# Kernel tuning notes

Measured on AMD Instinct MI355X. Metric: run time of the kernel, lower is better.

## Reference

```python
import jax, jax.numpy as jnp
import numpy as np
import math

N, CIN, DM, H, W = 4, 64, 32, 64, 64
KH = KW = 3

def setup_inputs() -> dict:
    key = jax.random.key(0)
    ks = jax.random.split(key, 12)
    sc = 0.05
    return {
        "h": jax.random.normal(ks[0], (N, CIN, H, W), jnp.float32),
        "m": jax.random.normal(ks[1], (N, CIN, H, W), jnp.float32),
        "Wh": jax.random.normal(ks[2], (3 * DM, CIN), jnp.float32) * sc,
        "bh": jax.random.normal(ks[3], (3 * DM,), jnp.float32) * sc,
        "Wm": jax.random.normal(ks[4], (2 * DM, CIN), jnp.float32) * sc,
        "bm": jax.random.normal(ks[5], (2 * DM,), jnp.float32) * sc,
        "Wz": jax.random.normal(ks[6], (DM, 2 * DM), jnp.float32) * sc,
        "bz": jax.random.normal(ks[7], (DM,), jnp.float32) * sc,
        "Wo": jax.random.normal(ks[8], (3 * CIN, CIN + DM, KH, KW), jnp.float32) * sc,
        "bo": jax.random.normal(ks[9], (3 * CIN,), jnp.float32) * sc,
    }

def _conv1x1(x, Wt, b):
    # x: [N,Ci,H,W], Wt: [Co,Ci] -> [N,Co,H,W]
    return jnp.einsum('oi,nihw->nohw', Wt, x) + b[None, :, None, None]

def _attend(q, k, v):
    # q,k,v: [N,C,S]; out: [N,C,S]
    C = q.shape[1]
    scores = jnp.einsum('ncs,nct->nst', q, k) / math.sqrt(C)  # [N,S,S]
    attn = jax.nn.softmax(scores, axis=-1)
    return jnp.einsum('nst,nct->ncs', attn, v)

def reference(h, m, Wh, bh, Wm, bm, Wz, bz, Wo, bo):
    n, _, hh, ww = h.shape
    S = hh * ww
    hq, hk, hv = jnp.split(_conv1x1(h, Wh, bh), 3, axis=1)
    mk, mv = jnp.split(_conv1x1(m, Wm, bm), 2, axis=1)
    hq = hq.reshape(n, DM, S)
    hk = hk.reshape(n, DM, S)
    hv = hv.reshape(n, DM, S)
    mk = mk.reshape(n, DM, S)
    mv = mv.reshape(n, DM, S)
    Zh = _attend(hq, hk, hv).reshape(n, DM, hh, ww)
    Zm = _attend(hq, mk, mv).reshape(n, DM, hh, ww)
    Z = _conv1x1(jnp.concatenate([Zh, Zm], axis=1), Wz, bz)
    x = jnp.concatenate([Z, h], axis=1)  # [N, DM+CIN, H, W]
    out = jax.lax.conv_general_dilated(
        x, Wo, window_strides=(1, 1), padding='SAME',
        dimension_numbers=('NCHW', 'OIHW', 'NCHW')) + bo[None, :, None, None]
    i, g, o = jnp.split(out, 3, axis=1)
    i = jax.nn.sigmoid(i)
    g = jnp.tanh(g)
    m_next = i * g + (1.0 - i) * m
    h_next = jax.nn.sigmoid(o) * m_next
    return (h_next, m_next)
```

## Files before the change

kernel.cpp:

```cpp
#include <hip/hip_runtime.h>
#include <math.h>

#define NB 4
#define CIN 64
#define DM 32
#define S 4096
#define NW 4

#define OFF_Q  0
#define OFF_KH 262144
#define OFF_VH 524288
#define OFF_KM 786432
#define OFF_VM 1048576
#define OFF_ZH 1310720
#define OFF_ZM 1572864
#define OFF_WF 1835008

typedef __attribute__((ext_vector_type(8))) short bf16x8;
typedef __attribute__((ext_vector_type(4))) short s16x4;
typedef __attribute__((ext_vector_type(4))) float f32x4;
typedef __attribute__((ext_vector_type(2))) unsigned int u32x2;
typedef __attribute__((ext_vector_type(4))) unsigned int u32x4;

__device__ inline unsigned short f2b(float x) {
  union { float f; unsigned u; } v;
  v.f = x;
  unsigned r = (v.u + 0x7FFF + ((v.u >> 16) & 1)) >> 16;
  return (unsigned short)r;
}

__device__ inline float b2f(unsigned short u) {
  union { unsigned u; float f; } v;
  v.u = ((unsigned)u) << 16;
  return v.f;
}

__device__ inline unsigned fbits(float x) {
  union { float f; unsigned u; } v;
  v.f = x;
  return v.u;
}

__global__ __launch_bounds__(256) void prep_kernel(
    const float* __restrict__ h, const float* __restrict__ m,
    const float* __restrict__ Wh, const float* __restrict__ bh,
    const float* __restrict__ Wm, const float* __restrict__ bm,
    const float* __restrict__ Wo, float* __restrict__ ws) {
  __shared__ unsigned short sm[64][34];
  int bid = blockIdx.x;
  int tid = threadIdx.x;

  if (bid >= 512) {
    int idx = (bid - 512) * 256 + tid;
    int f = idx >> 8;
    int r = idx & 255;
    int lane = r >> 2;
    int jp = (r & 3) * 2;
    int ql = lane & 15, quad = lane >> 4;
    int co = (f / 27) * 16 + ql;
    int k = (f % 27) * 32 + quad * 8 + jp;
    int tap = k / 96;
    int ci = k - tap * 96;
    float a = Wo[((size_t)co * 96 + ci) * 9 + tap];
    float b = Wo[((size_t)co * 96 + ci + 1) * 9 + tap];
    unsigned val = (unsigned)f2b(a) | ((unsigned)f2b(b) << 16);
    ((unsigned*)(ws + OFF_WF))[idx] = val;
    return;
  }

  int mode = (bid >= 256) ? 1 : 0;
  const float* in = mode ? m : h;
  const float* W = mode ? Wm : Wh;
  const float* b = mode ? bm : bh;
  int lbid = bid & 255;
  int n = lbid >> 6;
  int s0 = (lbid & 63) * 64;
  int sl = tid & 63;
  int cg = tid >> 6;
  const float* inp = in + (size_t)n * CIN * S + s0 + sl;

  float reg[64];
#pragma unroll
  for (int ci = 0; ci < 64; ++ci) reg[ci] = inp[(size_t)ci * S];

  float acc[24];
  int na = (mode == 0) ? 24 : 16;
  if (mode == 0) {
#pragma unroll
    for (int k = 0; k < 24; ++k) {
      int co = __builtin_amdgcn_readfirstlane(cg + k * 4);
      const float* w = W + (size_t)co * CIN;
      float a = b[co];
#pragma unroll
      for (int ci = 0; ci < CIN; ++ci) a += w[ci] * reg[ci];
      acc[k] = a;
    }
  } else {
#pragma unroll
    for (int k = 0; k < 16; ++k) {
      int co = __builtin_amdgcn_readfirstlane(cg + k * 4);
      const float* w = W + (size_t)co * CIN;
      float a = b[co];
#pragma unroll
      for (int ci = 0; ci < CIN; ++ci) a += w[ci] * reg[ci];
      acc[k] = a;
    }
  }
  (void)na;

  unsigned short* qsl = (unsigned short*)(ws + OFF_Q);
  unsigned short* khs = (unsigned short*)(ws + OFF_KH);
  unsigned short* vhs = (unsigned short*)(ws + OFF_VH);
  unsigned short* kms = (unsigned short*)(ws + OFF_KM);
  unsigned short* vms = (unsigned short*)(ws + OFF_VM);

  int ngrp = (mode == 0) ? 2 : 1;
  for (int g = 0; g < ngrp; ++g) {
    __syncthreads();
    const float rs = 0.2550400330665387f;
#pragma unroll
    for (int j = 0; j < 8; ++j) {
      int k = g * 8 + j;
      int c = cg + 4 * j;
      float v = acc[k];
      if (mode == 0 && g == 0) v *= rs;
      sm[sl][c] = f2b(v);
    }
    __syncthreads();
    unsigned short* dst;
    if (mode == 0)
      dst = (g == 0 ? qsl : khs);
    else
      dst = kms;
    unsigned* du = (unsigned*)(dst + ((size_t)n * S + s0) * 32);
#pragma unroll
    for (int i = 0; i < 4; ++i) {
      int idx = tid + i * 256;
      int s = idx >> 4, cp = idx & 15;
      unsigned val = (unsigned)sm[s][2 * cp] | ((unsigned)sm[s][2 * cp + 1] << 16);
      du[idx] = val;
    }
  }
  int k0 = (mode == 0) ? 16 : 8;
  unsigned short* vdst = (mode == 0) ? vhs : vms;
#pragma unroll
  for (int j = 0; j < 8; ++j) {
    int k = k0 + j;
    int c = cg + 4 * j;
    vdst[((size_t)n * DM + c) * S + s0 + sl] = f2b(acc[k]);
  }
}

union AttnSmem {
  unsigned short P[NW][2][1024];
  float osh[NW][2][32][16];
};

__global__ __launch_bounds__(256, 4) void attn_kernel(
    float* __restrict__ ws, const float* __restrict__ Wz,
    const float* __restrict__ bz) {
  __shared__ __align__(16) AttnSmem sm;
  __shared__ float lsh[NW][2][16];
  __shared__ unsigned short Olds[2][16][40];

  int bid = blockIdx.x;
  int ph = bid & 1;
  int n = (bid >> 1) & 3;
  int q0 = (bid >> 3) * 32;
  int tid = threadIdx.x;
  int w = tid >> 6;
  int lane = tid & 63;
  int ql = lane & 15;
  int quad = lane >> 4;
  int kbase = w * 1024;
  int sw = 2 * (ql & 7);

  const unsigned short* qs = (const unsigned short*)(ws + OFF_Q) + ((size_t)n * S + q0) * 32;
  const unsigned short* Ks = (const unsigned short*)(ws + (ph ? OFF_KM : OFF_KH)) + (size_t)n * S * 32;
  const unsigned short* Vs = (const unsigned short*)(ws + (ph ? OFF_VM : OFF_VH)) + (size_t)n * DM * S;
  unsigned short* Zp = (unsigned short*)(ws + (ph ? OFF_ZM : OFF_ZH)) + (size_t)n * DM * S;

  bf16x8 qf0 = *(const bf16x8*)(qs + ql * 32 + quad * 8);
  bf16x8 qf1 = *(const bf16x8*)(qs + (16 + ql) * 32 + quad * 8);

  f32x4 o00 = {0.f, 0.f, 0.f, 0.f}, o01 = {0.f, 0.f, 0.f, 0.f};
  f32x4 o10 = {0.f, 0.f, 0.f, 0.f}, o11 = {0.f, 0.f, 0.f, 0.f};
  f32x4 lsv0 = {0.f, 0.f, 0.f, 0.f}, lsv1 = {0.f, 0.f, 0.f, 0.f};
  const float ZI = -11.541560327111707f;
  const f32x4 zinit = {ZI, ZI, ZI, ZI};

  bf16x8 kfa[4], kfb[4];
#pragma unroll
  for (int t = 0; t < 4; ++t)
    kfa[t] = *(const bf16x8*)(Ks + (size_t)(kbase + t * 16 + ql) * 32 + quad * 8);

  auto step = [&](bf16x8 (&kfc)[4], bf16x8 (&kfn)[4], int kb, int kbn) {
    bf16x8 vf[4];
#pragma unroll
    for (int c2 = 0; c2 < 2; ++c2)
#pragma unroll
      for (int t2 = 0; t2 < 2; ++t2)
        vf[c2 * 2 + t2] = *(const bf16x8*)(Vs + (size_t)(t2 * 16 + ql) * S + kb + c2 * 32 + quad * 8);
#pragma unroll
    for (int t = 0; t < 4; ++t)
      kfn[t] = *(const bf16x8*)(Ks + (size_t)(kbn + t * 16 + ql) * 32 + quad * 8);

#pragma unroll
    for (int t = 0; t < 4; ++t) {
      f32x4 stt = __builtin_amdgcn_mfma_f32_16x16x32_bf16(kfc[t], qf0, zinit, 0, 0, 0);
      f32x4 e;
#pragma unroll
      for (int r = 0; r < 4; ++r) e[r] = __builtin_amdgcn_exp2f(stt[r]);
      lsv0 += e;
      u32x2 pk;
      pk[0] = __builtin_amdgcn_perm(fbits(e[1]), fbits(e[0]), 0x07060302u);
      pk[1] = __builtin_amdgcn_perm(fbits(e[3]), fbits(e[2]), 0x07060302u);
      *(u32x2*)(&sm.P[w][0][ql * 64 + ((t * 4 + quad) ^ sw) * 4]) = pk;
    }
#pragma unroll
    for (int t = 0; t < 4; ++t) {
      f32x4 stt = __builtin_amdgcn_mfma_f32_16x16x32_bf16(kfc[t], qf1, zinit, 0, 0, 0);
      f32x4 e;
#pragma unroll
      for (int r = 0; r < 4; ++r) e[r] = __builtin_amdgcn_exp2f(stt[r]);
      lsv1 += e;
      u32x2 pk;
      pk[0] = __builtin_amdgcn_perm(fbits(e[1]), fbits(e[0]), 0x07060302u);
      pk[1] = __builtin_amdgcn_perm(fbits(e[3]), fbits(e[2]), 0x07060302u);
      *(u32x2*)(&sm.P[w][1][ql * 64 + ((t * 4 + quad) ^ sw) * 4]) = pk;
    }

    __builtin_amdgcn_s_waitcnt(0xC07F);
    __builtin_amdgcn_wave_barrier();

#pragma unroll
    for (int c2 = 0; c2 < 2; ++c2) {
      bf16x8 pf0 = *(const bf16x8*)(&sm.P[w][0][ql * 64 + ((c2 * 8 + quad * 2) ^ sw) * 4]);
      bf16x8 pf1 = *(const bf16x8*)(&sm.P[w][1][ql * 64 + ((c2 * 8 + quad * 2) ^ sw) * 4]);
      o00 = __builtin_amdgcn_mfma_f32_16x16x32_bf16(vf[c2 * 2 + 0], pf0, o00, 0, 0, 0);
      o01 = __builtin_amdgcn_mfma_f32_16x16x32_bf16(vf[c2 * 2 + 1], pf0, o01, 0, 0, 0);
      o10 = __builtin_amdgcn_mfma_f32_16x16x32_bf16(vf[c2 * 2 + 0], pf1, o10, 0, 0, 0);
      o11 = __builtin_amdgcn_mfma_f32_16x16x32_bf16(vf[c2 * 2 + 1], pf1, o11, 0, 0, 0);
    }
    __builtin_amdgcn_wave_barrier();
  };

  for (int it = 0; it < 16; it += 2) {
    int kb0 = kbase + it * 64;
    int kb1 = kbase + ((it + 1) & 15) * 64;
    int kb2 = kbase + ((it + 2) & 15) * 64;
    step(kfa, kfb, kb0, kb1);
    step(kfb, kfa, kb1, kb2);
  }

  float lrun0 = lsv0[0] + lsv0[1] + lsv0[2] + lsv0[3];
  float lrun1 = lsv1[0] + lsv1[1] + lsv1[2] + lsv1[3];
  lrun0 += __shfl_xor(lrun0, 16);
  lrun0 += __shfl_xor(lrun0, 32);
  lrun1 += __shfl_xor(lrun1, 16);
  lrun1 += __shfl_xor(lrun1, 32);

  __syncthreads();
#pragma unroll
  for (int r = 0; r < 4; ++r) {
    sm.osh[w][0][quad * 4 + r][ql] = o00[r];
    sm.osh[w][0][16 + quad * 4 + r][ql] = o01[r];
    sm.osh[w][1][quad * 4 + r][ql] = o10[r];
    sm.osh[w][1][16 + quad * 4 + r][ql] = o11[r];
  }
  if (quad == 0) {
    lsh[w][0][ql] = lrun0;
    lsh[w][1][ql] = lrun1;
  }
  __syncthreads();

  if (w < 2) {
    int qt = w;
    float l = 0.f;
    f32x4 a0 = {0.f, 0.f, 0.f, 0.f}, a1 = {0.f, 0.f, 0.f, 0.f};
#pragma unroll
    for (int i = 0; i < NW; ++i) {
      l += lsh[i][qt][ql];
#pragma unroll
      for (int r = 0; r < 4; ++r) {
        a0[r] += sm.osh[i][qt][quad * 4 + r][ql];
        a1[r] += sm.osh[i][qt][16 + quad * 4 + r][ql];
      }
    }
    float inv = 1.0f / l;
    s16x4 w0, w1;
#pragma unroll
    for (int r = 0; r < 4; ++r) {
      w0[r] = (short)f2b(a0[r] * inv);
      w1[r] = (short)f2b(a1[r] * inv);
    }
    *(s16x4*)(&Olds[qt][ql][quad * 4]) = w0;
    *(s16x4*)(&Olds[qt][ql][16 + quad * 4]) = w1;
    __builtin_amdgcn_s_waitcnt(0xC07F);
    __builtin_amdgcn_wave_barrier();
    bf16x8 of = *(const bf16x8*)(&Olds[qt][ql][quad * 8]);

    const float* wzr0 = Wz + (size_t)ql * (2 * DM) + ph * DM + quad * 8;
    const float* wzr1 = Wz + (size_t)(ql + 16) * (2 * DM) + ph * DM + quad * 8;
    bf16x8 a0f, a1f;
#pragma unroll
    for (int j = 0; j < 8; ++j) {
      a0f[j] = (short)f2b(wzr0[j]);
      a1f[j] = (short)f2b(wzr1[j]);
    }
    f32x4 z0 = {0.f, 0.f, 0.f, 0.f}, z1 = {0.f, 0.f, 0.f, 0.f};
    if (ph == 0) {
#pragma unroll
      for (int r = 0; r < 4; ++r) {
        z0[r] = bz[quad * 4 + r];
        z1[r] = bz[16 + quad * 4 + r];
      }
    }
    z0 = __builtin_amdgcn_mfma_f32_16x16x32_bf16(a0f, of, z0, 0, 0, 0);
    z1 = __builtin_amdgcn_mfma_f32_16x16x32_bf16(a1f, of, z1, 0, 0, 0);
    int qc = q0 + qt * 16 + ql;
#pragma unroll
    for (int r = 0; r < 4; ++r) {
      Zp[(size_t)(quad * 4 + r) * S + qc] = f2b(z0[r]);
      Zp[(size_t)(16 + quad * 4 + r) * S + qc] = f2b(z1[r]);
    }
  }
}

__global__ __launch_bounds__(256) void conv_mfma_kernel(
    const float* __restrict__ ws, const float* __restrict__ h,
    const float* __restrict__ m, const float* __restrict__ bo,
    float* __restrict__ out) {
  __shared__ unsigned short xt[3][66][104];
  int bid = blockIdx.x;
  int n = bid >> 7;
  int rem = bid & 127;
  int g = rem & 1;
  int y = rem >> 1;
  int tid = threadIdx.x;
  int wv = tid >> 6;
  int lane = tid & 63;
  int ql = lane & 15, quad = lane >> 4;
  int x0 = wv * 16;

  const unsigned short* Zh = (const unsigned short*)(ws + OFF_ZH) + (size_t)n * DM * S;
  const unsigned short* Zm = (const unsigned short*)(ws + OFF_ZM) + (size_t)n * DM * S;
  const float* hb = h + (size_t)n * CIN * S;
  const unsigned short* Wf = (const unsigned short*)(ws + OFF_WF);

#pragma unroll
  for (int k = 0; k < 9; ++k) {
    int idx = tid + k * 256;
    int xm1 = idx & 63;
    int t2 = idx >> 6;
    int cb = t2 % 12;
    int r3 = t2 / 12;
    int yy = y + r3 - 1;
    u32x4 val = {0u, 0u, 0u, 0u};
    if (yy >= 0 && yy < 64) {
      int s = yy * 64 + xm1;
      int ci0 = cb * 8;
      float a[8];
      if (ci0 < 32) {
#pragma unroll
        for (int j = 0; j < 8; ++j)
          a[j] = b2f(Zh[(size_t)(ci0 + j) * S + s]) + b2f(Zm[(size_t)(ci0 + j) * S + s]);
      } else {
#pragma unroll
        for (int j = 0; j < 8; ++j)
          a[j] = hb[(size_t)(ci0 - 32 + j) * S + s];
      }
#pragma unroll
      for (int t = 0; t < 4; ++t)
        val[t] = (unsigned)f2b(a[2 * t]) | ((unsigned)f2b(a[2 * t + 1]) << 16);
    }
    *(u32x4*)(&xt[r3][xm1 + 1][cb * 8]) = val;
  }
  if (tid < 72) {
    int r3 = tid / 24;
    int rm = tid % 24;
    int side = rm / 12;
    int cb = rm % 12;
    *(u32x4*)(&xt[r3][side * 65][cb * 8]) = (u32x4){0u, 0u, 0u, 0u};
  }
  __syncthreads();

  f32x4 acc[6];
#pragma unroll
  for (int t = 0; t < 6; ++t) acc[t] = (f32x4){0.f, 0.f, 0.f, 0.f};

  const unsigned short* wfb[6];
#pragma unroll
  for (int j = 0; j < 6; ++j) {
    int t12 = (j >> 1) * 4 + g * 2 + (j & 1);
    wfb[j] = Wf + (size_t)t12 * 27 * 512 + lane * 8;
  }

#pragma unroll
  for (int dy = 0; dy < 3; ++dy) {
#pragma unroll
    for (int dx = 0; dx < 3; ++dx) {
      int tap = dy * 3 + dx;
#pragma unroll
      for (int cc = 0; cc < 3; ++cc) {
        bf16x8 b = *(const bf16x8*)(&xt[dy][x0 + ql + dx][cc * 32 + quad * 8]);
        int kb = tap * 3 + cc;
#pragma unroll
        for (int j = 0; j < 6; ++j) {
          bf16x8 wf = *(const bf16x8*)(wfb[j] + (size_t)kb * 512);
          acc[j] = __builtin_amdgcn_mfma_f32_16x16x32_bf16(wf, b, acc[j], 0, 0, 0);
        }
      }
    }
  }

  int s = y * 64 + x0 + ql;
#pragma unroll
  for (int jj = 0; jj < 2; ++jj) {
#pragma unroll
    for (int r = 0; r < 4; ++r) {
      int c = g * 32 + jj * 16 + quad * 4 + r;
      float iv = acc[jj][r] + bo[c];
      float gv = acc[2 + jj][r] + bo[64 + c];
      float ov = acc[4 + jj][r] + bo[128 + c];
      float ig = 1.f / (1.f + __expf(-iv));
      float gg = tanhf(gv);
      float og = 1.f / (1.f + __expf(-ov));
      size_t oidx = (((size_t)n * 64 + c) << 12) + s;
      float mold = m[oidx];
      float mn = ig * gg + (1.f - ig) * mold;
      out[oidx] = og * mn;
      out[(size_t)NB * CIN * S + oidx] = mn;
    }
  }
}

extern "C" void kernel_launch(void* const* d_in, const int* in_sizes, int n_in,
                              void* d_out, int out_size, void* d_ws, size_t ws_size,
                              hipStream_t stream) {
  const float* h = (const float*)d_in[0];
  const float* m = (const float*)d_in[1];
  const float* Wh = (const float*)d_in[2];
  const float* bh = (const float*)d_in[3];
  const float* Wm = (const float*)d_in[4];
  const float* bm = (const float*)d_in[5];
  const float* Wz = (const float*)d_in[6];
  const float* bz = (const float*)d_in[7];
  const float* Wo = (const float*)d_in[8];
  const float* bo = (const float*)d_in[9];
  float* out = (float*)d_out;
  float* ws = (float*)d_ws;

  prep_kernel<<<836, 256, 0, stream>>>(h, m, Wh, bh, Wm, bm, Wo, ws);
  attn_kernel<<<2 * NB * (S / 32), 256, 0, stream>>>(ws, Wz, bz);
  conv_mfma_kernel<<<NB * 128, 256, 0, stream>>>(ws, h, m, bo, out);
}
```

Measured before the change: 170.3 us.

## Restructure conv kernel: one block per row, split-K across waves, two x-fragments

The 3x3 conv kernel now uses 512 threads and one block per output row, covering both channel groups, so the input tile is staged once per row instead of twice. Each wave computes two 16-pixel fragments that share each weight load. The 27 K-blocks are split between two wave halves, and the partial sums are reduced through shared memory. The aim is to halve the redundant tile staging and improve weight reuse, at the cost of extra barriers, LDS for the reduction, and a grid of only 256 blocks.

```diff
diff --git a/kernel.cpp b/kernel.cpp
--- a/kernel.cpp
+++ b/kernel.cpp
@@ -84,7 +84,6 @@
   for (int ci = 0; ci < 64; ++ci) reg[ci] = inp[(size_t)ci * S];
 
   float acc[24];
-  int na = (mode == 0) ? 24 : 16;
   if (mode == 0) {
 #pragma unroll
     for (int k = 0; k < 24; ++k) {
@@ -106,7 +105,6 @@
       acc[k] = a;
     }
   }
-  (void)na;
 
   unsigned short* qsl = (unsigned short*)(ws + OFF_Q);
   unsigned short* khs = (unsigned short*)(ws + OFF_KH);
@@ -327,21 +325,23 @@
   }
 }
 
-__global__ __launch_bounds__(256) void conv_mfma_kernel(
+__global__ __launch_bounds__(512) void conv_mfma_kernel(
     const float* __restrict__ ws, const float* __restrict__ h,
     const float* __restrict__ m, const float* __restrict__ bo,
     float* __restrict__ out) {
-  __shared__ unsigned short xt[3][66][104];
+  __shared__ unsigned short xt[3][66][96];
+  __shared__ __align__(16) float mbuf[4][6][64][4];
   int bid = blockIdx.x;
-  int n = bid >> 7;
-  int rem = bid & 127;
-  int g = rem & 1;
-  int y = rem >> 1;
+  int n = bid >> 6;
+  int y = bid & 63;
   int tid = threadIdx.x;
-  int wv = tid >> 6;
+  int w = tid >> 6;
   int lane = tid & 63;
   int ql = lane & 15, quad = lane >> 4;
-  int x0 = wv * 16;
+  int kk = w >> 2;
+  int r2 = w & 3;
+  int g = r2 & 1;
+  int x0 = (r2 >> 1) * 32;
 
   const unsigned short* Zh = (const unsigned short*)(ws + OFF_ZH) + (size_t)n * DM * S;
   const unsigned short* Zm = (const unsigned short*)(ws + OFF_ZM) + (size_t)n * DM * S;
@@ -349,32 +349,34 @@
   const unsigned short* Wf = (const unsigned short*)(ws + OFF_WF);
 
 #pragma unroll
-  for (int k = 0; k < 9; ++k) {
-    int idx = tid + k * 256;
-    int xm1 = idx & 63;
-    int t2 = idx >> 6;
-    int cb = t2 % 12;
-    int r3 = t2 / 12;
-    int yy = y + r3 - 1;
-    u32x4 val = {0u, 0u, 0u, 0u};
-    if (yy >= 0 && yy < 64) {
-      int s = yy * 64 + xm1;
-      int ci0 = cb * 8;
-      float a[8];
-      if (ci0 < 32) {
-#pragma unroll
-        for (int j = 0; j < 8; ++j)
-          a[j] = b2f(Zh[(size_t)(ci0 + j) * S + s]) + b2f(Zm[(size_t)(ci0 + j) * S + s]);
-      } else {
-#pragma unroll
-        for (int j = 0; j < 8; ++j)
-          a[j] = hb[(size_t)(ci0 - 32 + j) * S + s];
+  for (int k = 0; k < 5; ++k) {
+    int idx = tid + k * 512;
+    if (idx < 2304) {
+      int xm1 = idx & 63;
+      int t2 = idx >> 6;
+      int cb = t2 % 12;
+      int r3 = t2 / 12;
+      int yy = y + r3 - 1;
+      u32x4 val = {0u, 0u, 0u, 0u};
+      if (yy >= 0 && yy < 64) {
+        int s = yy * 64 + xm1;
+        int ci0 = cb * 8;
+        float a[8];
+        if (ci0 < 32) {
+#pragma unroll
+          for (int j = 0; j < 8; ++j)
+            a[j] = b2f(Zh[(size_t)(ci0 + j) * S + s]) + b2f(Zm[(size_t)(ci0 + j) * S + s]);
+        } else {
+#pragma unroll
+          for (int j = 0; j < 8; ++j)
+            a[j] = hb[(size_t)(ci0 - 32 + j) * S + s];
+        }
+#pragma unroll
+        for (int t = 0; t < 4; ++t)
+          val[t] = (unsigned)f2b(a[2 * t]) | ((unsigned)f2b(a[2 * t + 1]) << 16);
       }
-#pragma unroll
-      for (int t = 0; t < 4; ++t)
-        val[t] = (unsigned)f2b(a[2 * t]) | ((unsigned)f2b(a[2 * t + 1]) << 16);
-    }
-    *(u32x4*)(&xt[r3][xm1 + 1][cb * 8]) = val;
+      *(u32x4*)(&xt[r3][xm1 + 1][cb * 8]) = val;
+    }
   }
   if (tid < 72) {
     int r3 = tid / 24;
@@ -385,9 +387,12 @@
   }
   __syncthreads();
 
-  f32x4 acc[6];
-#pragma unroll
-  for (int t = 0; t < 6; ++t) acc[t] = (f32x4){0.f, 0.f, 0.f, 0.f};
+  f32x4 acc0[6], acc1[6];
+#pragma unroll
+  for (int t = 0; t < 6; ++t) {
+    acc0[t] = (f32x4){0.f, 0.f, 0.f, 0.f};
+    acc1[t] = (f32x4){0.f, 0.f, 0.f, 0.f};
+  }
 
   const unsigned short* wfb[6];
 #pragma unroll
@@ -396,41 +401,64 @@
     wfb[j] = Wf + (size_t)t12 * 27 * 512 + lane * 8;
   }
 
-#pragma unroll
-  for (int dy = 0; dy < 3; ++dy) {
-#pragma unroll
-    for (int dx = 0; dx < 3; ++dx) {
-      int tap = dy * 3 + dx;
-#pragma unroll
-      for (int cc = 0; cc < 3; ++cc) {
-        bf16x8 b = *(const bf16x8*)(&xt[dy][x0 + ql + dx][cc * 32 + quad * 8]);
-        int kb = tap * 3 + cc;
-#pragma unroll
-        for (int j = 0; j < 6; ++j) {
-          bf16x8 wf = *(const bf16x8*)(wfb[j] + (size_t)kb * 512);
-          acc[j] = __builtin_amdgcn_mfma_f32_16x16x32_bf16(wf, b, acc[j], 0, 0, 0);
+  int kb_lo = kk * 14;
+  int kb_hi = kk ? 27 : 14;
+  for (int kb = kb_lo; kb < kb_hi; ++kb) {
+    int dy = kb / 9;
+    int rem = kb % 9;
+    int dx = rem / 3;
+    int cc = rem % 3;
+    bf16x8 b0 = *(const bf16x8*)(&xt[dy][x0 + ql + dx][cc * 32 + quad * 8]);
+    bf16x8 b1 = *(const bf16x8*)(&xt[dy][x0 + 16 + ql + dx][cc * 32 + quad * 8]);
+#pragma unroll
+    for (int j = 0; j < 6; ++j) {
+      bf16x8 wf = *(const bf16x8*)(wfb[j] + (size_t)kb * 512);
+      acc0[j] = __builtin_amdgcn_mfma_f32_16x16x32_bf16(wf, b0, acc0[j], 0, 0, 0);
+      acc1[j] = __builtin_amdgcn_mfma_f32_16x16x32_bf16(wf, b1, acc1[j], 0, 0, 0);
+    }
+  }
+
+  if (kk == 1) {
+#pragma unroll
+    for (int j = 0; j < 6; ++j) *(f32x4*)(&mbuf[r2][j][lane][0]) = acc0[j];
+  }
+  __syncthreads();
+  if (kk == 0) {
+#pragma unroll
+    for (int j = 0; j < 6; ++j) acc0[j] += *(const f32x4*)(&mbuf[r2][j][lane][0]);
+  }
+  __syncthreads();
+  if (kk == 1) {
+#pragma unroll
+    for (int j = 0; j < 6; ++j) *(f32x4*)(&mbuf[r2][j][lane][0]) = acc1[j];
+  }
+  __syncthreads();
+  if (kk == 0) {
+#pragma unroll
+    for (int j = 0; j < 6; ++j) acc1[j] += *(const f32x4*)(&mbuf[r2][j][lane][0]);
+
+#pragma unroll
+    for (int sfr = 0; sfr < 2; ++sfr) {
+      f32x4* ac = sfr ? acc1 : acc0;
+      int s = y * 64 + x0 + sfr * 16 + ql;
+#pragma unroll
+      for (int jj = 0; jj < 2; ++jj) {
+#pragma unroll
+        for (int r = 0; r < 4; ++r) {
+          int c = g * 32 + jj * 16 + quad * 4 + r;
+          float iv = ac[jj][r] + bo[c];
+          float gv = ac[2 + jj][r] + bo[64 + c];
+          float ov = ac[4 + jj][r] + bo[128 + c];
+          float ig = 1.f / (1.f + __expf(-iv));
+          float gg = tanhf(gv);
+          float og = 1.f / (1.f + __expf(-ov));
+          size_t oidx = (((size_t)n * 64 + c) << 12) + s;
+          float mold = m[oidx];
+          float mn = ig * gg + (1.f - ig) * mold;
+          out[oidx] = og * mn;
+          out[(size_t)NB * CIN * S + oidx] = mn;
         }
       }
-    }
-  }
-
-  int s = y * 64 + x0 + ql;
-#pragma unroll
-  for (int jj = 0; jj < 2; ++jj) {
-#pragma unroll
-    for (int r = 0; r < 4; ++r) {
-      int c = g * 32 + jj * 16 + quad * 4 + r;
-      float iv = acc[jj][r] + bo[c];
-      float gv = acc[2 + jj][r] + bo[64 + c];
-      float ov = acc[4 + jj][r] + bo[128 + c];
-      float ig = 1.f / (1.f + __expf(-iv));
-      float gg = tanhf(gv);
-      float og = 1.f / (1.f + __expf(-ov));
-      size_t oidx = (((size_t)n * 64 + c) << 12) + s;
-      float mold = m[oidx];
-      float mn = ig * gg + (1.f - ig) * mold;
-      out[oidx] = og * mn;
-      out[(size_t)NB * CIN * S + oidx] = mn;
     }
   }
 }
@@ -453,5 +481,5 @@
 
   prep_kernel<<<836, 256, 0, stream>>>(h, m, Wh, bh, Wm, bm, Wo, ws);
   attn_kernel<<<2 * NB * (S / 32), 256, 0, stream>>>(ws, Wz, bz);
-  conv_mfma_kernel<<<NB * 128, 256, 0, stream>>>(ws, h, m, bo, out);
-}
+  conv_mfma_kernel<<<NB * 64, 512, 0, stream>>>(ws, h, m, bo, out);
+}
```

Result: faster. 161.0 us (-5.4%).
